# Kernel tuning notes

Measured on AMD Instinct MI355X. Metric: run time of the kernel, lower is better.

## Reference

```python
import jax, jax.numpy as jnp
import numpy as np

B, N, D, YD = 256, 1024, 64, 2
EPS = 1e-7  # keras SCC epsilon clip


def interleave(x):
    # (B, L, ...): out[:,0::2]=first half, out[:,1::2]=second half
    b, L = x.shape[0], x.shape[1]
    a, c = x[:, : L // 2], x[:, L // 2:]
    return jnp.stack([a, c], axis=2).reshape((b, L) + x.shape[2:])


def block_interleave(x, scope):
    # tf.split into N//scope chunks of size `scope`, Interleave each, concat
    b, L = x.shape[0], x.shape[1]
    rest = x.shape[2:]
    xr = x.reshape((b, L // scope, 2, scope // 2) + rest)
    xr = jnp.swapaxes(xr, 2, 3)
    return xr.reshape((b, L) + rest)


def split_even_odd(x):
    # returns (odd, even) = (x[:,0::2], x[:,1::2])
    return x[:, 0::2], x[:, 1::2]


def mlp2(x, W1, b1, W2, b2):
    return jnp.dot(jax.nn.relu(jnp.dot(x, W1) + b1), W2) + b2


def emb2llr(e, W, b):
    return jax.nn.softmax(jnp.dot(e, W) + b, axis=-1)


def scce(v, p):
    # v: (B,L,1) int labels, p: (B,L,2) probs -> (B,L) per-element NLL
    pt = jnp.take_along_axis(p, v, axis=-1)[..., 0]
    return -jnp.log(jnp.clip(pt, EPS, 1.0))


def setup_inputs() -> dict:
    key = jax.random.key(0)
    ks = jax.random.split(key, 16)
    s = lambda fan: 1.0 / np.sqrt(fan)
    return {
        "x": jax.random.randint(ks[0], (B, N, 1), 0, 2, dtype=jnp.int32),
        "y": jax.random.normal(ks[1], (B, N, YD), dtype=jnp.float32),
        "emb_W": jax.random.normal(ks[2], (YD, D), dtype=jnp.float32) * s(YD),
        "emb_b": jnp.zeros((D,), jnp.float32),
        "lab_emb": jax.random.normal(ks[3], (2, D), dtype=jnp.float32) * s(D),
        "cn_W1": jax.random.normal(ks[4], (2 * D, D), dtype=jnp.float32) * s(2 * D),
        "cn_b1": jnp.zeros((D,), jnp.float32),
        "cn_W2": jax.random.normal(ks[5], (D, D), dtype=jnp.float32) * s(D),
        "cn_b2": jnp.zeros((D,), jnp.float32),
        "bn_W1": jax.random.normal(ks[6], (3 * D, D), dtype=jnp.float32) * s(3 * D),
        "bn_b1": jnp.zeros((D,), jnp.float32),
        "bn_W2": jax.random.normal(ks[7], (D, D), dtype=jnp.float32) * s(D),
        "bn_b2": jnp.zeros((D,), jnp.float32),
        "llr_W": jax.random.normal(ks[8], (D, 2), dtype=jnp.float32) * s(D),
        "llr_b": jnp.zeros((2,), jnp.float32),
    }


def reference(x, y, emb_W, emb_b, lab_emb, cn_W1, cn_b1, cn_W2, cn_b2,
              bn_W1, bn_b1, bn_W2, bn_b2, llr_W, llr_b):
    v = x.astype(jnp.int32)  # (B,N,1)
    e = jnp.dot(y, emb_W) + emb_b  # (B,N,D) observation embedding

    losses, preds, norms = [], [], []
    pred = emb2llr(e, llr_W, llr_b)
    losses.append(scce(v, pred))
    preds.append(pred)
    norms.append(jnp.linalg.norm(e, axis=-1))

    scope = 2
    while scope <= N:
        v_il = block_interleave(v, scope)
        v_odd, v_even = split_even_odd(v_il)
        v_xor = jnp.mod(v_odd + v_even, 2)  # (B,N/2,1)
        v_prime = interleave(jnp.concatenate((v_xor, v_even), axis=1))

        e_il = block_interleave(e, scope)
        e_odd, e_even = split_even_odd(e_il)  # (B,N/2,D) each
        v_xor_emb = lab_emb[v_xor[..., 0]]  # (B,N/2,D)

        e1_left = mlp2(jnp.concatenate((e_odd, e_even), axis=-1),
                       cn_W1, cn_b1, cn_W2, cn_b2)
        e1_right = mlp2(jnp.concatenate((e_odd, e_even, v_xor_emb), axis=-1),
                        bn_W1, bn_b1, bn_W2, bn_b2)
        e_prime = interleave(jnp.concatenate((e1_left, e1_right), axis=1))

        pred = emb2llr(e_prime, llr_W, llr_b)
        losses.append(scce(v_prime, pred))
        preds.append(pred)
        norms.append(jnp.linalg.norm(e_prime, axis=-1))

        v, e = v_prime, e_prime
        scope *= 2

    return (jnp.stack(losses, axis=-2),   # (B, S, N)
            jnp.stack(preds, axis=-2),    # (B, N, S, 2)
            jnp.stack(norms, axis=-2))    # (B, S, N)
```

## Files before the change

kernel.cpp:

```cpp
#include <hip/hip_runtime.h>
#include <hip/hip_bf16.h>

#define NB 256
#define NN 1024
#define NSTAGES 11
#define EPSF 1e-7f

typedef unsigned short u16;
typedef unsigned int u32;
typedef unsigned long long u64;
typedef __attribute__((ext_vector_type(8))) short short8;
typedef __attribute__((ext_vector_type(16))) float f32x16;

static constexpr size_t PRED_BASE = (size_t)NB * NSTAGES * NN;
static constexpr size_t NORM_BASE = PRED_BASE + (size_t)NB * NN * NSTAGES * 2;

static constexpr int LW_OFF = 24576;

#define WLDS_FR 30
#define NWREG (48 - WLDS_FR)

static constexpr size_t STAGE_OFF = 131072;
static constexpr size_t PRED_F2_PER_B = (size_t)NSTAGES * NN;

__device__ __forceinline__ u16 f2bf(float f) {
  unsigned u = __float_as_uint(f);
  unsigned r = (u + 0x7fffu + ((u >> 16) & 1u)) >> 16;
  return (u16)r;
}
__device__ __forceinline__ unsigned pack_bf2(float a, float b) {
  __hip_bfloat162 h = __float22bfloat162_rn(make_float2(a, b));
  return *(unsigned*)&h;
}
__device__ __forceinline__ u32 spread16(u32 v) {
  v = (v | (v << 8)) & 0x00FF00FFu;
  v = (v | (v << 4)) & 0x0F0F0F0Fu;
  v = (v | (v << 2)) & 0x33333333u;
  v = (v | (v << 1)) & 0x55555555u;
  return v;
}
template <bool STAGED>
__device__ __forceinline__ void emit_out(float* __restrict__ out, float* __restrict__ pred_ws,
                                         int b, int n, int s,
                                         float z0, float z1, float nrm2, int label) {
  float m  = fmaxf(z0, z1);
  float p0 = expf(z0 - m), p1 = expf(z1 - m);
  float inv = 1.0f / (p0 + p1);
  p0 *= inv; p1 *= inv;
  float pt = label ? p1 : p0;
  pt = fminf(fmaxf(pt, EPSF), 1.0f);
  out[((size_t)b * NSTAGES + s) * NN + n] = -logf(pt);
  if (STAGED) {
    ((float2*)pred_ws)[((size_t)b * NSTAGES + s) * NN + n] = make_float2(p0, p1);
  } else {
    size_t pb = PRED_BASE + (((size_t)b * NN + n) * NSTAGES + s) * 2;
    out[pb + 0] = p0;
    out[pb + 1] = p1;
  }
  out[NORM_BASE + ((size_t)b * NSTAGES + s) * NN + n] = sqrtf(nrm2);
}

__device__ __forceinline__ int eaddr(int row, int c16) {
  return row * 64 + (((c16) ^ (row & 7)) << 3);
}
__device__ __forceinline__ int eaddr32(int row, int m31) {
  return row * 64 + (((((m31) >> 2) ^ (row & 7)) << 3) | (((m31) & 3) << 1));
}

__global__ __launch_bounds__(256) void prep_kernel(
    const float* __restrict__ cn_W1, const float* __restrict__ bn_W1,
    const float* __restrict__ cn_W2, const float* __restrict__ bn_W2,
    const float* __restrict__ lab_emb, const float* __restrict__ llr_W,
    const float* __restrict__ bn_b1,
    u16* __restrict__ wfrag, float* __restrict__ labW_g) {
  int t = blockIdx.x * 256 + threadIdx.x;
  if (t < 3072) {
    int f = t >> 6, l = t & 63, h = l >> 5, c = l & 31;
    const float* src; int ks, nt;
    if (f < 16)      { src = cn_W1; ks = f >> 1; nt = f & 1; }
    else if (f < 32) { int g = f - 16; src = bn_W1; ks = g >> 1; nt = g & 1; }
    else if (f < 40) { int g = f - 32; src = cn_W2; ks = g >> 1; nt = g & 1; }
    else             { int g = f - 40; src = bn_W2; ks = g >> 1; nt = g & 1; }
    int col = 2 * c + nt;
    u16 vals[8];
    #pragma unroll
    for (int j = 0; j < 8; ++j) {
      int k = ks * 16 + h * 8 + j;
      vals[j] = f2bf(src[k * 64 + col]);
    }
    uint4 u;
    u.x = (unsigned)vals[0] | ((unsigned)vals[1] << 16);
    u.y = (unsigned)vals[2] | ((unsigned)vals[3] << 16);
    u.z = (unsigned)vals[4] | ((unsigned)vals[5] << 16);
    u.w = (unsigned)vals[6] | ((unsigned)vals[7] << 16);
    *(uint4*)(wfrag + (size_t)t * 8) = u;
  } else if (t < 3136) {
    int k = t - 3072;
    unsigned wv = (unsigned)f2bf(llr_W[k * 2]) | ((unsigned)f2bf(llr_W[k * 2 + 1]) << 16);
    ((unsigned*)(wfrag + LW_OFF))[k] = wv;
  } else if (t < 3264) {
    int idx = t - 3136;
    int v = idx >> 6, c = idx & 63;
    float acc = bn_b1[c];
    for (int d = 0; d < 64; ++d)
      acc = fmaf(lab_emb[v * 64 + d], bn_W1[(128 + d) * 64 + c], acc);
    labW_g[idx] = acc;
  }
}

__global__ __launch_bounds__(512) void pred_transpose_kernel(
    const float* __restrict__ pred_ws, float* __restrict__ out) {
  __shared__ float2 tb[NSTAGES * 1026];
  const int tid = threadIdx.x;
  const int b = blockIdx.x;
  const float2* src = (const float2*)pred_ws + (size_t)b * PRED_F2_PER_B;
  for (int i = tid; i < NSTAGES * NN; i += 512) {
    int s = i >> 10, n = i & (NN - 1);
    tb[s * 1026 + n] = src[i];
  }
  __syncthreads();
  float2* dst = (float2*)(out + PRED_BASE) + (size_t)b * PRED_F2_PER_B;
  for (int j = tid; j < NSTAGES * NN; j += 512) {
    int n = j / NSTAGES, s = j - n * NSTAGES;
    dst[j] = tb[s * 1026 + n];
  }
}

#define BFR(FI) (((FI) < WLDS_FR) ? *(const short8*)(wlds + (FI) * 512 + ln * 8) \
                                  : Wreg[(FI) - WLDS_FR])

template <int STAGED>
__global__ __launch_bounds__(512, 2) void polar_kernel(
    const int* __restrict__ x, const float* __restrict__ y,
    const float* __restrict__ emb_W, const float* __restrict__ emb_b,
    const u16* __restrict__ wfrag, const float* __restrict__ labW_g,
    const float* __restrict__ cn_b1, const float* __restrict__ cn_b2,
    const float* __restrict__ bn_b2, const float* __restrict__ llr_W,
    const float* __restrict__ llr_b, float* __restrict__ pred_ws,
    float* __restrict__ out) {
  __shared__ __align__(16) u16 eL[NN * 64];
  __shared__ __align__(16) u16 wlds[WLDS_FR * 512];
  __shared__ u32 lwL[64];
  __shared__ u32 vmask[2][32];
  __shared__ float labW[2][64];

  const int tid = threadIdx.x;
  const int w = tid >> 6, ln = tid & 63;
  const int m31 = ln & 31, h8 = ln >> 5;
  const int b = blockIdx.x;

  for (int i = tid; i < WLDS_FR * 64; i += 512)
    ((uint4*)wlds)[i] = ((const uint4*)wfrag)[i];
  if (tid < 64) lwL[tid] = ((const u32*)(wfrag + LW_OFF))[tid];
  if (tid < 128) ((float*)labW)[tid] = labW_g[tid];

  short8 Wreg[NWREG];
  #pragma unroll
  for (int fi = 0; fi < NWREG; ++fi)
    Wreg[fi] = *(const short8*)(wfrag + (size_t)(WLDS_FR + fi) * 512 + ln * 8);

  const float lb0 = llr_b[0], lb1 = llr_b[1];
  const float2 cb1 = *(const float2*)(cn_b1 + 2 * m31);
  const float2 cb2 = *(const float2*)(cn_b2 + 2 * m31);
  const float2 bb2 = *(const float2*)(bn_b2 + 2 * m31);

  #pragma unroll
  for (int rep = 0; rep < 2; ++rep) {
    int n = rep * 512 + tid;
    float2 yv = *(const float2*)(y + ((size_t)b * NN + n) * 2);
    float z0 = lb0, z1 = lb1, nr = 0.f;
    #pragma unroll
    for (int o8 = 0; o8 < 8; ++o8) {
      u32 vals[4];
      #pragma unroll
      for (int jj = 0; jj < 4; ++jj) {
        int o = o8 * 8 + jj * 2;
        float e0 = fmaf(yv.x, emb_W[o],     fmaf(yv.y, emb_W[64 + o],     emb_b[o]));
        float e1 = fmaf(yv.x, emb_W[o + 1], fmaf(yv.y, emb_W[64 + o + 1], emb_b[o + 1]));
        vals[jj] = pack_bf2(e0, e1);
        z0 = fmaf(e0, llr_W[o * 2 + 0], z0); z1 = fmaf(e0, llr_W[o * 2 + 1], z1);
        nr = fmaf(e0, e0, nr);
        z0 = fmaf(e1, llr_W[o * 2 + 2], z0); z1 = fmaf(e1, llr_W[o * 2 + 3], z1);
        nr = fmaf(e1, e1, nr);
      }
      uint4 q; q.x = vals[0]; q.y = vals[1]; q.z = vals[2]; q.w = vals[3];
      *(uint4*)(eL + eaddr(n, o8)) = q;
    }
    int v = x[(size_t)b * NN + n] & 1;
    emit_out<STAGED != 0>(out, pred_ws, b, n, 0, z0, z1, nr, v);
    u64 bm = __ballot(v != 0);
    if (ln == 0)  vmask[0][rep * 16 + 2 * w]     = (u32)bm;
    if (ln == 32) vmask[0][rep * 16 + 2 * w + 1] = (u32)(bm >> 32);
  }
  __syncthreads();

  const float2 lwv0 = *(const float2*)(&labW[0][2 * m31]);
  const float2 lwv1 = *(const float2*)(&labW[1][2 * m31]);

  #pragma unroll 1
  for (int s = 1; s <= 10; ++s) {
    const int sh = s - 1;
    const int half = 1 << sh;
    const u32* vmR = vmask[(s - 1) & 1];
    u32* vmW = vmask[s & 1];

    short8 Ao[2][4], Ae[2][4];
    int io[2], ie[2], vo[2], ve[2], vx[2];
    u32 bxs[2];
    #pragma unroll
    for (int t = 0; t < 2; ++t) {
      int i = 64 * w + 32 * t + m31;
      int g = i >> sh, u = i & (half - 1);
      io[t] = g * (half << 1) + u;
      ie[t] = io[t] + half;
      #pragma unroll
      for (int f = 0; f < 4; ++f) {
        Ao[t][f] = *(const short8*)(eL + eaddr(io[t], f * 2 + h8));
        Ae[t][f] = *(const short8*)(eL + eaddr(ie[t], f * 2 + h8));
      }
      vo[t] = (vmR[io[t] >> 5] >> (io[t] & 31)) & 1;
      ve[t] = (vmR[ie[t] >> 5] >> (ie[t] & 31)) & 1;
      vx[t] = vo[t] ^ ve[t];
      u32 bx = (u32)__ballot(vx[t] != 0);
      u32 be = (u32)__ballot(ve[t] != 0);
      bxs[t] = bx;
      u32 lo = spread16(bx & 0xffffu) | (spread16(be & 0xffffu) << 1);
      u32 hi = spread16(bx >> 16) | (spread16(be >> 16) << 1);
      if (ln == 0) { vmW[4 * w + 2 * t] = lo; vmW[4 * w + 2 * t + 1] = hi; }
    }
    __syncthreads();

    if (s >= 2) {
      const uint4* lwq = (const uint4*)lwL;
      uint4 lq[4][2];
      #pragma unroll
      for (int f = 0; f < 4; ++f) {
        lq[f][0] = lwq[f * 4 + h8 * 2];
        lq[f][1] = lwq[f * 4 + h8 * 2 + 1];
      }
      #pragma unroll
      for (int t = 0; t < 2; ++t) {
        #pragma unroll
        for (int side = 0; side < 2; ++side) {
          float z0 = 0.f, z1 = 0.f, nr = 0.f;
          #pragma unroll
          for (int f = 0; f < 4; ++f) {
            short8 av8 = side ? Ae[t][f] : Ao[t][f];
            #pragma unroll
            for (int j = 0; j < 8; ++j) {
              u32 pv = ((const u32*)&av8)[j >> 1];
              float val = __uint_as_float((j & 1) ? (pv & 0xffff0000u) : (pv << 16));
              u32 lwp = (j < 4) ? ((const u32*)&lq[f][0])[j] : ((const u32*)&lq[f][1])[j - 4];
              z0 = fmaf(val, __uint_as_float(lwp << 16), z0);
              z1 = fmaf(val, __uint_as_float(lwp & 0xffff0000u), z1);
              nr = fmaf(val, val, nr);
            }
          }
          z0 += __shfl_xor(z0, 32);
          z1 += __shfl_xor(z1, 32);
          nr += __shfl_xor(nr, 32);
          if (h8 == 0)
            emit_out<STAGED != 0>(out, pred_ws, b, side ? ie[t] : io[t], s - 1,
                                  z0 + lb0, z1 + lb1, nr, side ? ve[t] : vo[t]);
        }
      }
    }

    f32x16 a0[2], a1[2];
    #pragma unroll
    for (int t = 0; t < 2; ++t)
      #pragma unroll
      for (int r = 0; r < 16; ++r) { a0[t][r] = cb1.x; a1[t][r] = cb1.y; }
    #pragma unroll
    for (int ks = 0; ks < 8; ++ks) {
      short8 B0 = BFR(ks * 2 + 0);
      short8 B1 = BFR(ks * 2 + 1);
      #pragma unroll
      for (int t = 0; t < 2; ++t) {
        short8 a = (ks < 4) ? Ao[t][ks] : Ae[t][ks - 4];
        a0[t] = __builtin_amdgcn_mfma_f32_32x32x16_bf16(a, B0, a0[t], 0, 0, 0);
        a1[t] = __builtin_amdgcn_mfma_f32_32x32x16_bf16(a, B1, a1[t], 0, 0, 0);
      }
    }
    #pragma unroll
    for (int t = 0; t < 2; ++t) {
      int obase = 128 * w + 64 * t;
      #pragma unroll
      for (int r = 0; r < 16; ++r) {
        int row = (r & 3) + 8 * (r >> 2) + 4 * h8;
        int R = obase + 2 * row;
        *(u32*)(eL + eaddr32(R, m31)) =
            pack_bf2(fmaxf(a0[t][r], 0.f), fmaxf(a1[t][r], 0.f));
      }
    }

    #pragma unroll
    for (int t = 0; t < 2; ++t)
      #pragma unroll
      for (int r = 0; r < 16; ++r) {
        int row = (r & 3) + 8 * (r >> 2) + 4 * h8;
        int bit = (bxs[t] >> row) & 1;
        a0[t][r] = bit ? lwv1.x : lwv0.x;
        a1[t][r] = bit ? lwv1.y : lwv0.y;
      }
    #pragma unroll
    for (int ks = 0; ks < 8; ++ks) {
      short8 B0 = BFR(16 + ks * 2 + 0);
      short8 B1 = BFR(16 + ks * 2 + 1);
      #pragma unroll
      for (int t = 0; t < 2; ++t) {
        short8 a = (ks < 4) ? Ao[t][ks] : Ae[t][ks - 4];
        a0[t] = __builtin_amdgcn_mfma_f32_32x32x16_bf16(a, B0, a0[t], 0, 0, 0);
        a1[t] = __builtin_amdgcn_mfma_f32_32x32x16_bf16(a, B1, a1[t], 0, 0, 0);
      }
    }
    #pragma unroll
    for (int t = 0; t < 2; ++t) {
      int obase = 128 * w + 64 * t;
      #pragma unroll
      for (int r = 0; r < 16; ++r) {
        int row = (r & 3) + 8 * (r >> 2) + 4 * h8;
        int R = obase + 2 * row + 1;
        *(u32*)(eL + eaddr32(R, m31)) =
            pack_bf2(fmaxf(a0[t][r], 0.f), fmaxf(a1[t][r], 0.f));
      }
    }

    {
      short8 Hc[2][4];
      #pragma unroll
      for (int t = 0; t < 2; ++t) {
        int R = 128 * w + 64 * t + 2 * m31;
        #pragma unroll
        for (int f = 0; f < 4; ++f)
          Hc[t][f] = *(const short8*)(eL + eaddr(R, f * 2 + h8));
      }
      f32x16 d0[2], d1[2];
      #pragma unroll
      for (int t = 0; t < 2; ++t)
        #pragma unroll
        for (int r = 0; r < 16; ++r) { d0[t][r] = cb2.x; d1[t][r] = cb2.y; }
      #pragma unroll
      for (int ks = 0; ks < 4; ++ks) {
        short8 B0 = BFR(32 + ks * 2 + 0);
        short8 B1 = BFR(32 + ks * 2 + 1);
        #pragma unroll
        for (int t = 0; t < 2; ++t) {
          d0[t] = __builtin_amdgcn_mfma_f32_32x32x16_bf16(Hc[t][ks], B0, d0[t], 0, 0, 0);
          d1[t] = __builtin_amdgcn_mfma_f32_32x32x16_bf16(Hc[t][ks], B1, d1[t], 0, 0, 0);
        }
      }
      #pragma unroll
      for (int t = 0; t < 2; ++t) {
        int obase = 128 * w + 64 * t;
        #pragma unroll
        for (int r = 0; r < 16; ++r) {
          int row = (r & 3) + 8 * (r >> 2) + 4 * h8;
          int R = obase + 2 * row;
          *(u32*)(eL + eaddr32(R, m31)) = pack_bf2(d0[t][r], d1[t][r]);
        }
      }
    }

    {
      short8 Hb[2][4];
      #pragma unroll
      for (int t = 0; t < 2; ++t) {
        int R = 128 * w + 64 * t + 2 * m31 + 1;
        #pragma unroll
        for (int f = 0; f < 4; ++f)
          Hb[t][f] = *(const short8*)(eL + eaddr(R, f * 2 + h8));
      }
      f32x16 d0[2], d1[2];
      #pragma unroll
      for (int t = 0; t < 2; ++t)
        #pragma unroll
        for (int r = 0; r < 16; ++r) { d0[t][r] = bb2.x; d1[t][r] = bb2.y; }
      #pragma unroll
      for (int ks = 0; ks < 4; ++ks) {
        short8 B0 = BFR(40 + ks * 2 + 0);
        short8 B1 = BFR(40 + ks * 2 + 1);
        #pragma unroll
        for (int t = 0; t < 2; ++t) {
          d0[t] = __builtin_amdgcn_mfma_f32_32x32x16_bf16(Hb[t][ks], B0, d0[t], 0, 0, 0);
          d1[t] = __builtin_amdgcn_mfma_f32_32x32x16_bf16(Hb[t][ks], B1, d1[t], 0, 0, 0);
        }
      }
      #pragma unroll
      for (int t = 0; t < 2; ++t) {
        int obase = 128 * w + 64 * t;
        #pragma unroll
        for (int r = 0; r < 16; ++r) {
          int row = (r & 3) + 8 * (r >> 2) + 4 * h8;
          int R = obase + 2 * row + 1;
          *(u32*)(eL + eaddr32(R, m31)) = pack_bf2(d0[t][r], d1[t][r]);
        }
      }
    }
    __syncthreads();
  }

  {
    const uint4* lwq = (const uint4*)lwL;
    uint4 lq[4][2];
    #pragma unroll
    for (int f = 0; f < 4; ++f) {
      lq[f][0] = lwq[f * 4 + h8 * 2];
      lq[f][1] = lwq[f * 4 + h8 * 2 + 1];
    }
    #pragma unroll
    for (int it = 0; it < 4; ++it) {
      int n = 128 * w + 32 * it + m31;
      float z0 = 0.f, z1 = 0.f, nr = 0.f;
      #pragma unroll
      for (int f = 0; f < 4; ++f) {
        short8 av8 = *(const short8*)(eL + eaddr(n, f * 2 + h8));
        #pragma unroll
        for (int j = 0; j < 8; ++j) {
          u32 pv = ((const u32*)&av8)[j >> 1];
          float val = __uint_as_float((j & 1) ? (pv & 0xffff0000u) : (pv << 16));
          u32 lwp = (j < 4) ? ((const u32*)&lq[f][0])[j] : ((const u32*)&lq[f][1])[j - 4];
          z0 = fmaf(val, __uint_as_float(lwp << 16), z0);
          z1 = fmaf(val, __uint_as_float(lwp & 0xffff0000u), z1);
          nr = fmaf(val, val, nr);
        }
      }
      z0 += __shfl_xor(z0, 32);
      z1 += __shfl_xor(z1, 32);
      nr += __shfl_xor(nr, 32);
      int lab = (vmask[0][n >> 5] >> (n & 31)) & 1;
      if (h8 == 0)
        emit_out<STAGED != 0>(out, pred_ws, b, n, NSTAGES - 1, z0 + lb0, z1 + lb1, nr, lab);
    }
  }
}

extern "C" void kernel_launch(void* const* d_in, const int* in_sizes, int n_in,
                              void* d_out, int out_size, void* d_ws, size_t ws_size,
                              hipStream_t stream) {
  const int*   x      = (const int*)d_in[0];
  const float* y      = (const float*)d_in[1];
  const float* emb_W  = (const float*)d_in[2];
  const float* emb_b  = (const float*)d_in[3];
  const float* labemb = (const float*)d_in[4];
  const float* cn_W1  = (const float*)d_in[5];
  const float* cn_b1  = (const float*)d_in[6];
  const float* cn_W2  = (const float*)d_in[7];
  const float* cn_b2  = (const float*)d_in[8];
  const float* bn_W1  = (const float*)d_in[9];
  const float* bn_b1  = (const float*)d_in[10];
  const float* bn_W2  = (const float*)d_in[11];
  const float* bn_b2  = (const float*)d_in[12];
  const float* llr_W  = (const float*)d_in[13];
  const float* llr_b  = (const float*)d_in[14];
  float* out = (float*)d_out;

  u16* wfrag = (u16*)d_ws;
  float* labW_g = (float*)((char*)d_ws + 65536);
  float* pred_ws = (float*)((char*)d_ws + STAGE_OFF);
  size_t need = STAGE_OFF + (size_t)NB * NSTAGES * NN * 2 * sizeof(float);

  prep_kernel<<<13, 256, 0, stream>>>(cn_W1, bn_W1, cn_W2, bn_W2, labemb, llr_W,
                                      bn_b1, wfrag, labW_g);
  if (ws_size >= need) {
    polar_kernel<1><<<NB, 512, 0, stream>>>(x, y, emb_W, emb_b, wfrag, labW_g,
                                            cn_b1, cn_b2, bn_b2, llr_W, llr_b,
                                            pred_ws, out);
    pred_transpose_kernel<<<NB, 512, 0, stream>>>(pred_ws, out);
  } else {
    polar_kernel<0><<<NB, 512, 0, stream>>>(x, y, emb_W, emb_b, wfrag, labW_g,
                                            cn_b1, cn_b2, bn_b2, llr_W, llr_b,
                                            pred_ws, out);
  }
}
```

Before: 265.2 us.

## Split polar decoder into two half-sequence blocks per batch for early stages

Stages 0-9 now run in a kernel that launches two blocks per batch row, each owning 512 of the 1024 positions. This works because block interleaving at scopes up to 512 stays inside each half. The intermediate embeddings and label masks are written to workspace, and a second per-batch kernel finishes the final full-length stage. The intent is to double the number of blocks to fill more compute units and to keep all weight fragments in LDS instead of registers. The cost is an extra global round trip of the embeddings, one more kernel launch, and a larger workspace requirement.

After: 252.8 us, median of 2. -4.7%, faster.

```diff
diff --git a/kernel.cpp b/kernel.cpp
--- a/kernel.cpp
+++ b/kernel.cpp
@@ -18,10 +18,15 @@
 static constexpr int LW_OFF = 24576;
 
 #define WLDS_FR 30
-#define NWREG (48 - WLDS_FR)
 
 static constexpr size_t STAGE_OFF = 131072;
 static constexpr size_t PRED_F2_PER_B = (size_t)NSTAGES * NN;
+static constexpr size_t PRED_BYTES = (size_t)NB * NSTAGES * NN * 2 * sizeof(float);
+static constexpr size_t E9_OFF = STAGE_OFF + PRED_BYTES;
+static constexpr size_t E9_BYTES = (size_t)512 * 65536;
+static constexpr size_t VM_OFF = E9_OFF + E9_BYTES;
+static constexpr size_t NEED_SPLIT = VM_OFF + (size_t)512 * 16 * sizeof(u32);
+static constexpr size_t NEED_STAGED = STAGE_OFF + PRED_BYTES;
 
 __device__ __forceinline__ u16 f2bf(float f) {
   unsigned u = __float_as_uint(f);
@@ -126,11 +131,517 @@
   }
 }
 
+#define AFR(FI) (*(const short8*)(wlds + (FI) * 512 + ln * 8))
 #define BFR(FI) (((FI) < WLDS_FR) ? *(const short8*)(wlds + (FI) * 512 + ln * 8) \
-                                  : Wreg[(FI) - WLDS_FR])
+                                  : *(const short8*)(wfrag + (size_t)(FI) * 512 + ln * 8))
+
+__global__ __launch_bounds__(512, 2) void polar_a_kernel(
+    const int* __restrict__ x, const float* __restrict__ y,
+    const float* __restrict__ emb_W, const float* __restrict__ emb_b,
+    const u16* __restrict__ wfrag, const float* __restrict__ labW_g,
+    const float* __restrict__ cn_b1, const float* __restrict__ cn_b2,
+    const float* __restrict__ bn_b2, const float* __restrict__ llr_W,
+    const float* __restrict__ llr_b, float* __restrict__ pred_ws,
+    u16* __restrict__ e9_ws, u32* __restrict__ vm_ws,
+    float* __restrict__ out) {
+  __shared__ __align__(16) u16 eLh[512 * 64];
+  __shared__ __align__(16) u16 wlds[48 * 512];
+  __shared__ u32 lwL[64];
+  __shared__ u32 vmask[2][16];
+  __shared__ float labW[2][64];
+
+  const int tid = threadIdx.x;
+  const int w = tid >> 6, ln = tid & 63;
+  const int m31 = ln & 31, h8 = ln >> 5;
+  const int b = blockIdx.x >> 1, h = blockIdx.x & 1;
+
+  for (int i = tid; i < 48 * 64; i += 512)
+    ((uint4*)wlds)[i] = ((const uint4*)wfrag)[i];
+  if (tid < 64) lwL[tid] = ((const u32*)(wfrag + LW_OFF))[tid];
+  if (tid < 128) ((float*)labW)[tid] = labW_g[tid];
+
+  const float lb0 = llr_b[0], lb1 = llr_b[1];
+  const float2 cb1 = *(const float2*)(cn_b1 + 2 * m31);
+  const float2 cb2 = *(const float2*)(cn_b2 + 2 * m31);
+  const float2 bb2 = *(const float2*)(bn_b2 + 2 * m31);
+
+  {
+    int nl = tid;
+    int n = 512 * h + nl;
+    float2 yv = *(const float2*)(y + ((size_t)b * NN + n) * 2);
+    float z0 = lb0, z1 = lb1, nr = 0.f;
+    #pragma unroll
+    for (int o8 = 0; o8 < 8; ++o8) {
+      u32 vals[4];
+      #pragma unroll
+      for (int jj = 0; jj < 4; ++jj) {
+        int o = o8 * 8 + jj * 2;
+        float e0 = fmaf(yv.x, emb_W[o],     fmaf(yv.y, emb_W[64 + o],     emb_b[o]));
+        float e1 = fmaf(yv.x, emb_W[o + 1], fmaf(yv.y, emb_W[64 + o + 1], emb_b[o + 1]));
+        vals[jj] = pack_bf2(e0, e1);
+        z0 = fmaf(e0, llr_W[o * 2 + 0], z0); z1 = fmaf(e0, llr_W[o * 2 + 1], z1);
+        nr = fmaf(e0, e0, nr);
+        z0 = fmaf(e1, llr_W[o * 2 + 2], z0); z1 = fmaf(e1, llr_W[o * 2 + 3], z1);
+        nr = fmaf(e1, e1, nr);
+      }
+      uint4 q; q.x = vals[0]; q.y = vals[1]; q.z = vals[2]; q.w = vals[3];
+      *(uint4*)(eLh + eaddr(nl, o8)) = q;
+    }
+    int v = x[(size_t)b * NN + n] & 1;
+    emit_out<true>(out, pred_ws, b, n, 0, z0, z1, nr, v);
+    u64 bm = __ballot(v != 0);
+    if (ln == 0)  vmask[0][2 * w]     = (u32)bm;
+    if (ln == 32) vmask[0][2 * w + 1] = (u32)(bm >> 32);
+  }
+  __syncthreads();
+
+  const float2 lwv0 = *(const float2*)(&labW[0][2 * m31]);
+  const float2 lwv1 = *(const float2*)(&labW[1][2 * m31]);
+
+  #pragma unroll 1
+  for (int s = 1; s <= 9; ++s) {
+    const int sh = s - 1;
+    const int half = 1 << sh;
+    const u32* vmR = vmask[(s - 1) & 1];
+    u32* vmW = vmask[s & 1];
+
+    short8 Ao[4], Ae[4];
+    int iog, ieg, iol, iel, vo, ve, vx;
+    u32 bxs;
+    {
+      int i = 256 * h + 32 * w + m31;
+      int g = i >> sh, u = i & (half - 1);
+      iog = g * (half << 1) + u;
+      ieg = iog + half;
+      iol = iog & 511; iel = ieg & 511;
+      #pragma unroll
+      for (int f = 0; f < 4; ++f) {
+        Ao[f] = *(const short8*)(eLh + eaddr(iol, f * 2 + h8));
+        Ae[f] = *(const short8*)(eLh + eaddr(iel, f * 2 + h8));
+      }
+      vo = (vmR[iol >> 5] >> (iol & 31)) & 1;
+      ve = (vmR[iel >> 5] >> (iel & 31)) & 1;
+      vx = vo ^ ve;
+      u32 bx = (u32)__ballot(vx != 0);
+      u32 be = (u32)__ballot(ve != 0);
+      bxs = bx;
+      u32 lo = spread16(bx & 0xffffu) | (spread16(be & 0xffffu) << 1);
+      u32 hi = spread16(bx >> 16) | (spread16(be >> 16) << 1);
+      if (ln == 0) { vmW[2 * w] = lo; vmW[2 * w + 1] = hi; }
+    }
+    __syncthreads();
+
+    if (s >= 2) {
+      const uint4* lwq = (const uint4*)lwL;
+      uint4 lq[4][2];
+      #pragma unroll
+      for (int f = 0; f < 4; ++f) {
+        lq[f][0] = lwq[f * 4 + h8 * 2];
+        lq[f][1] = lwq[f * 4 + h8 * 2 + 1];
+      }
+      #pragma unroll
+      for (int side = 0; side < 2; ++side) {
+        float z0 = 0.f, z1 = 0.f, nr = 0.f;
+        #pragma unroll
+        for (int f = 0; f < 4; ++f) {
+          short8 av8 = side ? Ae[f] : Ao[f];
+          #pragma unroll
+          for (int j = 0; j < 8; ++j) {
+            u32 pv = ((const u32*)&av8)[j >> 1];
+            float val = __uint_as_float((j & 1) ? (pv & 0xffff0000u) : (pv << 16));
+            u32 lwp = (j < 4) ? ((const u32*)&lq[f][0])[j] : ((const u32*)&lq[f][1])[j - 4];
+            z0 = fmaf(val, __uint_as_float(lwp << 16), z0);
+            z1 = fmaf(val, __uint_as_float(lwp & 0xffff0000u), z1);
+            nr = fmaf(val, val, nr);
+          }
+        }
+        z0 += __shfl_xor(z0, 32);
+        z1 += __shfl_xor(z1, 32);
+        nr += __shfl_xor(nr, 32);
+        if (h8 == 0)
+          emit_out<true>(out, pred_ws, b, side ? ieg : iog, s - 1,
+                         z0 + lb0, z1 + lb1, nr, side ? ve : vo);
+      }
+    }
+
+    f32x16 a0, a1;
+    #pragma unroll
+    for (int r = 0; r < 16; ++r) { a0[r] = cb1.x; a1[r] = cb1.y; }
+    #pragma unroll
+    for (int ks = 0; ks < 8; ++ks) {
+      short8 B0 = AFR(ks * 2 + 0);
+      short8 B1 = AFR(ks * 2 + 1);
+      short8 a = (ks < 4) ? Ao[ks] : Ae[ks - 4];
+      a0 = __builtin_amdgcn_mfma_f32_32x32x16_bf16(a, B0, a0, 0, 0, 0);
+      a1 = __builtin_amdgcn_mfma_f32_32x32x16_bf16(a, B1, a1, 0, 0, 0);
+    }
+    {
+      int obase = 64 * w;
+      #pragma unroll
+      for (int r = 0; r < 16; ++r) {
+        int row = (r & 3) + 8 * (r >> 2) + 4 * h8;
+        int R = obase + 2 * row;
+        *(u32*)(eLh + eaddr32(R, m31)) =
+            pack_bf2(fmaxf(a0[r], 0.f), fmaxf(a1[r], 0.f));
+      }
+    }
+
+    #pragma unroll
+    for (int r = 0; r < 16; ++r) {
+      int row = (r & 3) + 8 * (r >> 2) + 4 * h8;
+      int bit = (bxs >> row) & 1;
+      a0[r] = bit ? lwv1.x : lwv0.x;
+      a1[r] = bit ? lwv1.y : lwv0.y;
+    }
+    #pragma unroll
+    for (int ks = 0; ks < 8; ++ks) {
+      short8 B0 = AFR(16 + ks * 2 + 0);
+      short8 B1 = AFR(16 + ks * 2 + 1);
+      short8 a = (ks < 4) ? Ao[ks] : Ae[ks - 4];
+      a0 = __builtin_amdgcn_mfma_f32_32x32x16_bf16(a, B0, a0, 0, 0, 0);
+      a1 = __builtin_amdgcn_mfma_f32_32x32x16_bf16(a, B1, a1, 0, 0, 0);
+    }
+    {
+      int obase = 64 * w;
+      #pragma unroll
+      for (int r = 0; r < 16; ++r) {
+        int row = (r & 3) + 8 * (r >> 2) + 4 * h8;
+        int R = obase + 2 * row + 1;
+        *(u32*)(eLh + eaddr32(R, m31)) =
+            pack_bf2(fmaxf(a0[r], 0.f), fmaxf(a1[r], 0.f));
+      }
+    }
+
+    {
+      short8 Hc[4];
+      {
+        int R = 64 * w + 2 * m31;
+        #pragma unroll
+        for (int f = 0; f < 4; ++f)
+          Hc[f] = *(const short8*)(eLh + eaddr(R, f * 2 + h8));
+      }
+      f32x16 d0, d1;
+      #pragma unroll
+      for (int r = 0; r < 16; ++r) { d0[r] = cb2.x; d1[r] = cb2.y; }
+      #pragma unroll
+      for (int ks = 0; ks < 4; ++ks) {
+        short8 B0 = AFR(32 + ks * 2 + 0);
+        short8 B1 = AFR(32 + ks * 2 + 1);
+        d0 = __builtin_amdgcn_mfma_f32_32x32x16_bf16(Hc[ks], B0, d0, 0, 0, 0);
+        d1 = __builtin_amdgcn_mfma_f32_32x32x16_bf16(Hc[ks], B1, d1, 0, 0, 0);
+      }
+      int obase = 64 * w;
+      #pragma unroll
+      for (int r = 0; r < 16; ++r) {
+        int row = (r & 3) + 8 * (r >> 2) + 4 * h8;
+        int R = obase + 2 * row;
+        *(u32*)(eLh + eaddr32(R, m31)) = pack_bf2(d0[r], d1[r]);
+      }
+    }
+
+    {
+      short8 Hb[4];
+      {
+        int R = 64 * w + 2 * m31 + 1;
+        #pragma unroll
+        for (int f = 0; f < 4; ++f)
+          Hb[f] = *(const short8*)(eLh + eaddr(R, f * 2 + h8));
+      }
+      f32x16 d0, d1;
+      #pragma unroll
+      for (int r = 0; r < 16; ++r) { d0[r] = bb2.x; d1[r] = bb2.y; }
+      #pragma unroll
+      for (int ks = 0; ks < 4; ++ks) {
+        short8 B0 = AFR(40 + ks * 2 + 0);
+        short8 B1 = AFR(40 + ks * 2 + 1);
+        d0 = __builtin_amdgcn_mfma_f32_32x32x16_bf16(Hb[ks], B0, d0, 0, 0, 0);
+        d1 = __builtin_amdgcn_mfma_f32_32x32x16_bf16(Hb[ks], B1, d1, 0, 0, 0);
+      }
+      int obase = 64 * w;
+      #pragma unroll
+      for (int r = 0; r < 16; ++r) {
+        int row = (r & 3) + 8 * (r >> 2) + 4 * h8;
+        int R = obase + 2 * row + 1;
+        *(u32*)(eLh + eaddr32(R, m31)) = pack_bf2(d0[r], d1[r]);
+      }
+    }
+    __syncthreads();
+  }
+
+  {
+    const uint4* src = (const uint4*)eLh;
+    uint4* dst = (uint4*)(e9_ws + (size_t)(b * 2 + h) * 32768);
+    for (int i = tid; i < 4096; i += 512) dst[i] = src[i];
+    if (tid < 16) vm_ws[(b * 2 + h) * 16 + tid] = vmask[1][tid];
+  }
+}
+
+__global__ __launch_bounds__(512, 2) void polar_b_kernel(
+    const u16* __restrict__ wfrag, const float* __restrict__ labW_g,
+    const float* __restrict__ cn_b1, const float* __restrict__ cn_b2,
+    const float* __restrict__ bn_b2, const float* __restrict__ llr_b,
+    float* __restrict__ pred_ws, const u16* __restrict__ e9_ws,
+    const u32* __restrict__ vm_ws, float* __restrict__ out) {
+  __shared__ __align__(16) u16 eL[NN * 64];
+  __shared__ __align__(16) u16 wlds[WLDS_FR * 512];
+  __shared__ u32 lwL[64];
+  __shared__ u32 vmA[32];
+  __shared__ u32 vmB[32];
+  __shared__ float labW[2][64];
+
+  const int tid = threadIdx.x;
+  const int w = tid >> 6, ln = tid & 63;
+  const int m31 = ln & 31, h8 = ln >> 5;
+  const int b = blockIdx.x;
+
+  for (int i = tid; i < WLDS_FR * 64; i += 512)
+    ((uint4*)wlds)[i] = ((const uint4*)wfrag)[i];
+  if (tid < 64) lwL[tid] = ((const u32*)(wfrag + LW_OFF))[tid];
+  if (tid < 128) ((float*)labW)[tid] = labW_g[tid];
+  if (tid < 32) vmA[tid] = vm_ws[b * 32 + tid];
+
+  const float lb0 = llr_b[0], lb1 = llr_b[1];
+  const float2 cb1 = *(const float2*)(cn_b1 + 2 * m31);
+  const float2 cb2 = *(const float2*)(cn_b2 + 2 * m31);
+  const float2 bb2 = *(const float2*)(bn_b2 + 2 * m31);
+  __syncthreads();
+
+  const float2 lwv0 = *(const float2*)(&labW[0][2 * m31]);
+  const float2 lwv1 = *(const float2*)(&labW[1][2 * m31]);
+
+  const u16* e9a = e9_ws + (size_t)(b * 2 + 0) * 32768;
+  const u16* e9b = e9_ws + (size_t)(b * 2 + 1) * 32768;
+
+  short8 Ao[2][4], Ae[2][4];
+  int io[2], ie[2], vo[2], ve[2], vx[2];
+  u32 bxs[2];
+  #pragma unroll
+  for (int t = 0; t < 2; ++t) {
+    int i = 64 * w + 32 * t + m31;
+    io[t] = i; ie[t] = i + 512;
+    #pragma unroll
+    for (int f = 0; f < 4; ++f) {
+      Ao[t][f] = *(const short8*)(e9a + eaddr(i, f * 2 + h8));
+      Ae[t][f] = *(const short8*)(e9b + eaddr(i, f * 2 + h8));
+    }
+    vo[t] = (vmA[i >> 5] >> (i & 31)) & 1;
+    ve[t] = (vmA[(i >> 5) + 16] >> (i & 31)) & 1;
+    vx[t] = vo[t] ^ ve[t];
+    u32 bx = (u32)__ballot(vx[t] != 0);
+    u32 be = (u32)__ballot(ve[t] != 0);
+    bxs[t] = bx;
+    u32 lo = spread16(bx & 0xffffu) | (spread16(be & 0xffffu) << 1);
+    u32 hi = spread16(bx >> 16) | (spread16(be >> 16) << 1);
+    if (ln == 0) { vmB[4 * w + 2 * t] = lo; vmB[4 * w + 2 * t + 1] = hi; }
+  }
+  __syncthreads();
+
+  {
+    const uint4* lwq = (const uint4*)lwL;
+    uint4 lq[4][2];
+    #pragma unroll
+    for (int f = 0; f < 4; ++f) {
+      lq[f][0] = lwq[f * 4 + h8 * 2];
+      lq[f][1] = lwq[f * 4 + h8 * 2 + 1];
+    }
+    #pragma unroll
+    for (int t = 0; t < 2; ++t) {
+      #pragma unroll
+      for (int side = 0; side < 2; ++side) {
+        float z0 = 0.f, z1 = 0.f, nr = 0.f;
+        #pragma unroll
+        for (int f = 0; f < 4; ++f) {
+          short8 av8 = side ? Ae[t][f] : Ao[t][f];
+          #pragma unroll
+          for (int j = 0; j < 8; ++j) {
+            u32 pv = ((const u32*)&av8)[j >> 1];
+            float val = __uint_as_float((j & 1) ? (pv & 0xffff0000u) : (pv << 16));
+            u32 lwp = (j < 4) ? ((const u32*)&lq[f][0])[j] : ((const u32*)&lq[f][1])[j - 4];
+            z0 = fmaf(val, __uint_as_float(lwp << 16), z0);
+            z1 = fmaf(val, __uint_as_float(lwp & 0xffff0000u), z1);
+            nr = fmaf(val, val, nr);
+          }
+        }
+        z0 += __shfl_xor(z0, 32);
+        z1 += __shfl_xor(z1, 32);
+        nr += __shfl_xor(nr, 32);
+        if (h8 == 0)
+          emit_out<true>(out, pred_ws, b, side ? ie[t] : io[t], 9,
+                         z0 + lb0, z1 + lb1, nr, side ? ve[t] : vo[t]);
+      }
+    }
+  }
+
+  f32x16 a0[2], a1[2];
+  #pragma unroll
+  for (int t = 0; t < 2; ++t)
+    #pragma unroll
+    for (int r = 0; r < 16; ++r) { a0[t][r] = cb1.x; a1[t][r] = cb1.y; }
+  #pragma unroll
+  for (int ks = 0; ks < 8; ++ks) {
+    short8 B0 = BFR(ks * 2 + 0);
+    short8 B1 = BFR(ks * 2 + 1);
+    #pragma unroll
+    for (int t = 0; t < 2; ++t) {
+      short8 a = (ks < 4) ? Ao[t][ks] : Ae[t][ks - 4];
+      a0[t] = __builtin_amdgcn_mfma_f32_32x32x16_bf16(a, B0, a0[t], 0, 0, 0);
+      a1[t] = __builtin_amdgcn_mfma_f32_32x32x16_bf16(a, B1, a1[t], 0, 0, 0);
+    }
+  }
+  #pragma unroll
+  for (int t = 0; t < 2; ++t) {
+    int obase = 128 * w + 64 * t;
+    #pragma unroll
+    for (int r = 0; r < 16; ++r) {
+      int row = (r & 3) + 8 * (r >> 2) + 4 * h8;
+      int R = obase + 2 * row;
+      *(u32*)(eL + eaddr32(R, m31)) =
+          pack_bf2(fmaxf(a0[t][r], 0.f), fmaxf(a1[t][r], 0.f));
+    }
+  }
+
+  #pragma unroll
+  for (int t = 0; t < 2; ++t)
+    #pragma unroll
+    for (int r = 0; r < 16; ++r) {
+      int row = (r & 3) + 8 * (r >> 2) + 4 * h8;
+      int bit = (bxs[t] >> row) & 1;
+      a0[t][r] = bit ? lwv1.x : lwv0.x;
+      a1[t][r] = bit ? lwv1.y : lwv0.y;
+    }
+  #pragma unroll
+  for (int ks = 0; ks < 8; ++ks) {
+    short8 B0 = BFR(16 + ks * 2 + 0);
+    short8 B1 = BFR(16 + ks * 2 + 1);
+    #pragma unroll
+    for (int t = 0; t < 2; ++t) {
+      short8 a = (ks < 4) ? Ao[t][ks] : Ae[t][ks - 4];
+      a0[t] = __builtin_amdgcn_mfma_f32_32x32x16_bf16(a, B0, a0[t], 0, 0, 0);
+      a1[t] = __builtin_amdgcn_mfma_f32_32x32x16_bf16(a, B1, a1[t], 0, 0, 0);
+    }
+  }
+  #pragma unroll
+  for (int t = 0; t < 2; ++t) {
+    int obase = 128 * w + 64 * t;
+    #pragma unroll
+    for (int r = 0; r < 16; ++r) {
+      int row = (r & 3) + 8 * (r >> 2) + 4 * h8;
+      int R = obase + 2 * row + 1;
+      *(u32*)(eL + eaddr32(R, m31)) =
+          pack_bf2(fmaxf(a0[t][r], 0.f), fmaxf(a1[t][r], 0.f));
+    }
+  }
+
+  {
+    short8 Hc[2][4];
+    #pragma unroll
+    for (int t = 0; t < 2; ++t) {
+      int R = 128 * w + 64 * t + 2 * m31;
+      #pragma unroll
+      for (int f = 0; f < 4; ++f)
+        Hc[t][f] = *(const short8*)(eL + eaddr(R, f * 2 + h8));
+    }
+    f32x16 d0[2], d1[2];
+    #pragma unroll
+    for (int t = 0; t < 2; ++t)
+      #pragma unroll
+      for (int r = 0; r < 16; ++r) { d0[t][r] = cb2.x; d1[t][r] = cb2.y; }
+    #pragma unroll
+    for (int ks = 0; ks < 4; ++ks) {
+      short8 B0 = BFR(32 + ks * 2 + 0);
+      short8 B1 = BFR(32 + ks * 2 + 1);
+      #pragma unroll
+      for (int t = 0; t < 2; ++t) {
+        d0[t] = __builtin_amdgcn_mfma_f32_32x32x16_bf16(Hc[t][ks], B0, d0[t], 0, 0, 0);
+        d1[t] = __builtin_amdgcn_mfma_f32_32x32x16_bf16(Hc[t][ks], B1, d1[t], 0, 0, 0);
+      }
+    }
+    #pragma unroll
+    for (int t = 0; t < 2; ++t) {
+      int obase = 128 * w + 64 * t;
+      #pragma unroll
+      for (int r = 0; r < 16; ++r) {
+        int row = (r & 3) + 8 * (r >> 2) + 4 * h8;
+        int R = obase + 2 * row;
+        *(u32*)(eL + eaddr32(R, m31)) = pack_bf2(d0[t][r], d1[t][r]);
+      }
+    }
+  }
+
+  {
+    short8 Hb[2][4];
+    #pragma unroll
+    for (int t = 0; t < 2; ++t) {
+      int R = 128 * w + 64 * t + 2 * m31 + 1;
+      #pragma unroll
+      for (int f = 0; f < 4; ++f)
+        Hb[t][f] = *(const short8*)(eL + eaddr(R, f * 2 + h8));
+    }
+    f32x16 d0[2], d1[2];
+    #pragma unroll
+    for (int t = 0; t < 2; ++t)
+      #pragma unroll
+      for (int r = 0; r < 16; ++r) { d0[t][r] = bb2.x; d1[t][r] = bb2.y; }
+    #pragma unroll
+    for (int ks = 0; ks < 4; ++ks) {
+      short8 B0 = BFR(40 + ks * 2 + 0);
+      short8 B1 = BFR(40 + ks * 2 + 1);
+      #pragma unroll
+      for (int t = 0; t < 2; ++t) {
+        d0[t] = __builtin_amdgcn_mfma_f32_32x32x16_bf16(Hb[t][ks], B0, d0[t], 0, 0, 0);
+        d1[t] = __builtin_amdgcn_mfma_f32_32x32x16_bf16(Hb[t][ks], B1, d1[t], 0, 0, 0);
+      }
+    }
+    #pragma unroll
+    for (int t = 0; t < 2; ++t) {
+      int obase = 128 * w + 64 * t;
+      #pragma unroll
+      for (int r = 0; r < 16; ++r) {
+        int row = (r & 3) + 8 * (r >> 2) + 4 * h8;
+        int R = obase + 2 * row + 1;
+        *(u32*)(eL + eaddr32(R, m31)) = pack_bf2(d0[t][r], d1[t][r]);
+      }
+    }
+  }
+  __syncthreads();
+
+  {
+    const uint4* lwq = (const uint4*)lwL;
+    uint4 lq[4][2];
+    #pragma unroll
+    for (int f = 0; f < 4; ++f) {
+      lq[f][0] = lwq[f * 4 + h8 * 2];
+      lq[f][1] = lwq[f * 4 + h8 * 2 + 1];
+    }
+    #pragma unroll
+    for (int it = 0; it < 4; ++it) {
+      int n = 128 * w + 32 * it + m31;
+      float z0 = 0.f, z1 = 0.f, nr = 0.f;
+      #pragma unroll
+      for (int f = 0; f < 4; ++f) {
+        short8 av8 = *(const short8*)(eL + eaddr(n, f * 2 + h8));
+        #pragma unroll
+        for (int j = 0; j < 8; ++j) {
+          u32 pv = ((const u32*)&av8)[j >> 1];
+          float val = __uint_as_float((j & 1) ? (pv & 0xffff0000u) : (pv << 16));
+          u32 lwp = (j < 4) ? ((const u32*)&lq[f][0])[j] : ((const u32*)&lq[f][1])[j - 4];
+          z0 = fmaf(val, __uint_as_float(lwp << 16), z0);
+          z1 = fmaf(val, __uint_as_float(lwp & 0xffff0000u), z1);
+          nr = fmaf(val, val, nr);
+        }
+      }
+      z0 += __shfl_xor(z0, 32);
+      z1 += __shfl_xor(z1, 32);
+      nr += __shfl_xor(nr, 32);
+      int lab = (vmB[n >> 5] >> (n & 31)) & 1;
+      if (h8 == 0)
+        emit_out<true>(out, pred_ws, b, n, NSTAGES - 1, z0 + lb0, z1 + lb1, nr, lab);
+    }
+  }
+}
 
 template <int STAGED>
-__global__ __launch_bounds__(512, 2) void polar_kernel(
+__global__ __launch_bounds__(512, 2) void polar_mono_kernel(
     const int* __restrict__ x, const float* __restrict__ y,
     const float* __restrict__ emb_W, const float* __restrict__ emb_b,
     const u16* __restrict__ wfrag, const float* __restrict__ labW_g,
@@ -153,11 +664,6 @@
     ((uint4*)wlds)[i] = ((const uint4*)wfrag)[i];
   if (tid < 64) lwL[tid] = ((const u32*)(wfrag + LW_OFF))[tid];
   if (tid < 128) ((float*)labW)[tid] = labW_g[tid];
-
-  short8 Wreg[NWREG];
-  #pragma unroll
-  for (int fi = 0; fi < NWREG; ++fi)
-    Wreg[fi] = *(const short8*)(wfrag + (size_t)(WLDS_FR + fi) * 512 + ln * 8);
 
   const float lb0 = llr_b[0], lb1 = llr_b[1];
   const float2 cb1 = *(const float2*)(cn_b1 + 2 * m31);
@@ -458,18 +964,26 @@
   u16* wfrag = (u16*)d_ws;
   float* labW_g = (float*)((char*)d_ws + 65536);
   float* pred_ws = (float*)((char*)d_ws + STAGE_OFF);
-  size_t need = STAGE_OFF + (size_t)NB * NSTAGES * NN * 2 * sizeof(float);
+  u16* e9_ws = (u16*)((char*)d_ws + E9_OFF);
+  u32* vm_ws = (u32*)((char*)d_ws + VM_OFF);
 
   prep_kernel<<<13, 256, 0, stream>>>(cn_W1, bn_W1, cn_W2, bn_W2, labemb, llr_W,
                                       bn_b1, wfrag, labW_g);
-  if (ws_size >= need) {
-    polar_kernel<1><<<NB, 512, 0, stream>>>(x, y, emb_W, emb_b, wfrag, labW_g,
-                                            cn_b1, cn_b2, bn_b2, llr_W, llr_b,
-                                            pred_ws, out);
+  if (ws_size >= NEED_SPLIT) {
+    polar_a_kernel<<<2 * NB, 512, 0, stream>>>(x, y, emb_W, emb_b, wfrag, labW_g,
+                                               cn_b1, cn_b2, bn_b2, llr_W, llr_b,
+                                               pred_ws, e9_ws, vm_ws, out);
+    polar_b_kernel<<<NB, 512, 0, stream>>>(wfrag, labW_g, cn_b1, cn_b2, bn_b2,
+                                           llr_b, pred_ws, e9_ws, vm_ws, out);
+    pred_transpose_kernel<<<NB, 512, 0, stream>>>(pred_ws, out);
+  } else if (ws_size >= NEED_STAGED) {
+    polar_mono_kernel<1><<<NB, 512, 0, stream>>>(x, y, emb_W, emb_b, wfrag, labW_g,
+                                                 cn_b1, cn_b2, bn_b2, llr_W, llr_b,
+                                                 pred_ws, out);
     pred_transpose_kernel<<<NB, 512, 0, stream>>>(pred_ws, out);
   } else {
-    polar_kernel<0><<<NB, 512, 0, stream>>>(x, y, emb_W, emb_b, wfrag, labW_g,
-                                            cn_b1, cn_b2, bn_b2, llr_W, llr_b,
-                                            pred_ws, out);
-  }
-}
+    polar_mono_kernel<0><<<NB, 512, 0, stream>>>(x, y, emb_W, emb_b, wfrag, labW_g,
+                                                 cn_b1, cn_b2, bn_b2, llr_W, llr_b,
+                                                 pred_ws, out);
+  }
+}
```
